# Performance work log

Hardware: AMD Instinct MI355X
Metric: run time of the kernel (lower is better)

Reference implementation:

```python
import jax, jax.numpy as jnp
import numpy as np

# Static conv hyperparameters (match init_kwargs)
STRIDE = (1, 1)
PAD = (1, 1)
DIL = (1, 1)
GROUPS = 1
DG = 1  # num_deformable_groups


def setup_inputs() -> dict:
    key = jax.random.key(0)
    k1, k2, k3 = jax.random.split(key, 3)
    B, C, H, W = 4, 256, 64, 64
    OC, kh, kw = 256, 3, 3
    x = jax.random.normal(k1, (B, C, H, W), dtype=jnp.float32)
    # offset: [B, DG*2*kh*kw, Ho, Wo], ordered (tap, [dy, dx]) per deformable group
    offset = jax.random.normal(k2, (B, DG * 2 * kh * kw, H, W), dtype=jnp.float32)
    n = C * kh * kw
    stdv = 1.0 / np.sqrt(n)
    weight = jax.random.uniform(k3, (OC, C // GROUPS, kh, kw), dtype=jnp.float32,
                                minval=-stdv, maxval=stdv)
    return {"x": x, "offset": offset, "weight": weight}


def _deform_conv(x, offset, weight):
    B, C, H, W = x.shape
    OC, Cg_w, kh, kw = weight.shape
    sh, sw = STRIDE
    ph, pw = PAD
    dh, dw = DIL
    Ho = (H + 2 * ph - (dh * (kh - 1) + 1)) // sh + 1
    Wo = (W + 2 * pw - (dw * (kw - 1) + 1)) // sw + 1
    K = kh * kw
    Cg = C // DG  # channels per deformable group

    # offsets: [B, DG, K, 2, Ho, Wo]; channel 0 = dy (h), channel 1 = dx (w)
    off = offset.reshape(B, DG, K, 2, Ho, Wo)

    # base (undeformed) sampling positions per tap
    ki, kj = jnp.meshgrid(jnp.arange(kh), jnp.arange(kw), indexing='ij')
    base_h = (jnp.arange(Ho) * sh - ph)[None, :] + (ki.reshape(-1) * dh)[:, None]  # [K, Ho]
    base_w = (jnp.arange(Wo) * sw - pw)[None, :] + (kj.reshape(-1) * dw)[:, None]  # [K, Wo]

    pos_h = base_h[None, None, :, :, None].astype(x.dtype) + off[:, :, :, 0]  # [B,DG,K,Ho,Wo]
    pos_w = base_w[None, None, :, None, :].astype(x.dtype) + off[:, :, :, 1]  # [B,DG,K,Ho,Wo]

    h0f = jnp.floor(pos_h)
    w0f = jnp.floor(pos_w)
    lh = pos_h - h0f  # fractional parts
    lw = pos_w - w0f
    h0 = h0f.astype(jnp.int32)
    w0 = w0f.astype(jnp.int32)

    xg = x.reshape(B, DG, Cg, H * W)

    def gather(hi, wi):
        # zero-padded gather: out-of-range corners contribute 0 (mmcv DCNv1 semantics)
        valid = (hi >= 0) & (hi < H) & (wi >= 0) & (wi < W)  # [B,DG,K,Ho,Wo]
        idx = jnp.clip(hi, 0, H - 1) * W + jnp.clip(wi, 0, W - 1)
        flat = idx.reshape(B, DG, 1, K * Ho * Wo)
        vals = jnp.take_along_axis(
            xg, jnp.broadcast_to(flat, (B, DG, Cg, K * Ho * Wo)), axis=3)
        vals = vals.reshape(B, DG, Cg, K, Ho, Wo)
        return vals * valid[:, :, None].astype(x.dtype)

    # bilinear interpolation over 4 corners -> im2col columns [B,DG,Cg,K,Ho,Wo]
    cols = (gather(h0, w0) * ((1 - lh) * (1 - lw))[:, :, None]
            + gather(h0, w0 + 1) * ((1 - lh) * lw)[:, :, None]
            + gather(h0 + 1, w0) * (lh * (1 - lw))[:, :, None]
            + gather(h0 + 1, w0 + 1) * (lh * lw)[:, :, None])

    # grouped GEMM: columns x weight
    cols = cols.reshape(B, GROUPS, C // GROUPS, K, Ho, Wo)
    wg = weight.reshape(GROUPS, OC // GROUPS, Cg_w, K)
    out = jnp.einsum('gock,bgckhw->bgohw', wg, cols)
    return out.reshape(B, OC, Ho, Wo)


def reference(x, offset, weight):
    return _deform_conv(x, offset, weight)
```

## Files before the change

kernel.cpp:

```cpp
#include <hip/hip_runtime.h>
#include <hip/hip_bf16.h>
#include <math.h>


constexpr int B  = 4;
constexpr int C  = 256;
constexpr int H  = 64;
constexpr int W  = 64;
constexpr int OC = 256;
constexpr int Ho = 64;
constexpr int Wo = 64;

constexpr int NT     = 64;
constexpr int CHUNKS = 72;
constexpr int WROW   = 40;

constexpr size_t WA_ELTS  = (size_t)CHUNKS * OC * WROW;
constexpr size_t XB_ELTS  = (size_t)B * 8 * 4096 * 32;
constexpr size_t OUT_ELTS = (size_t)B * OC * Ho * Wo;

typedef __attribute__((ext_vector_type(8))) short bf16x8;
typedef __attribute__((ext_vector_type(4))) float f32x4;

__device__ __forceinline__ float bf_lo(unsigned u) {
    union { unsigned i; float f; } c; c.i = u << 16; return c.f;
}
__device__ __forceinline__ float bf_hi(unsigned u) {
    union { unsigned i; float f; } c; c.i = u & 0xffff0000u; return c.f;
}
__device__ __forceinline__ ushort fbf(float f) {
    __hip_bfloat16 h = __float2bfloat16(f); return *(ushort*)&h;
}

__global__ __launch_bounds__(256)
void prep_all(const float* __restrict__ x, const float* __restrict__ wt,
              ushort* __restrict__ xb, ushort* __restrict__ wA)
{
    __shared__ ushort sx[128 * WROW];
    __shared__ ushort sw[CHUNKS * WROW];
    const int t = threadIdx.x;

    if (blockIdx.x < 1024) {
        const int blk = blockIdx.x;
        const int hwb = blk & 31;
        const int cb  = (blk >> 5) & 7;
        const int b   = blk >> 8;
        const int hw0 = hwb << 7;
        const int lhw = t & 127, chalf = t >> 7;
        #pragma unroll
        for (int i = 0; i < 16; ++i) {
            const int c = i * 2 + chalf;
            sx[lhw * WROW + c] =
                fbf(x[(((size_t)(b * 256 + cb * 32 + c)) << 12) + hw0 + lhw]);
        }
        __syncthreads();
        const int whw = t >> 1, wh = t & 1;
        const uint4 v0 = *(const uint4*)&sx[whw * WROW + wh * 16];
        const uint4 v1 = *(const uint4*)&sx[whw * WROW + wh * 16 + 8];
        uint4* dst = (uint4*)(xb + ((size_t)((b * 8 + cb) * 4096 + hw0) << 5));
        dst[whw * 4 + wh * 2 + 0] = v0;
        dst[whw * 4 + wh * 2 + 1] = v1;
    } else {
        const int oc = blockIdx.x - 1024;
        const int c  = t, chb = c >> 5, kk = c & 31;
        const float* wp = wt + ((size_t)oc * C + c) * 9;
        #pragma unroll
        for (int tap = 0; tap < 9; ++tap)
            sw[(tap * 8 + chb) * WROW + kk] = fbf(wp[tap]);
        if (c < CHUNKS) {
            #pragma unroll
            for (int j = 0; j < 8; ++j) sw[c * WROW + 32 + j] = 0;
        }
        __syncthreads();
        const uint4* sv = (const uint4*)sw;
        for (int i = c; i < CHUNKS * 5; i += 256) {
            const int row = i / 5, q = i % 5;
            ((uint4*)(wA + ((size_t)row * OC + oc) * WROW))[q] = sv[i];
        }
    }
}

struct GathRegs { uint4 c00, c01, c10, c11; float4 mw; };

__global__ __launch_bounds__(512, 4)
void dcn_mfma(const ushort* __restrict__ xb, const float* __restrict__ off,
              const ushort* __restrict__ wA_g, float* __restrict__ po)
{
    __shared__ __align__(16) ushort s_wA[2][OC * WROW];
    __shared__ __align__(16) ushort s_col[2][NT * WROW];
    __shared__ __align__(16) float4 s_mw[9 * NT];
    __shared__ __align__(8)  int2   s_midx[9 * NT];

    const int xcd = blockIdx.x & 7;
    const int ii  = blockIdx.x >> 3;
    const int b   = xcd & 3;
    const int khalf = ii & 1;
    const int ho  = ((xcd >> 2) << 5) + (ii >> 1);
    const int ch0 = khalf * 36;
    float* outp = po + (size_t)khalf * OUT_ELTS;
    const int tid = threadIdx.x;

    for (int s = tid; s < 9 * NT; s += 512) {
        const int n   = s & 63;
        const int tap = s >> 6;
        const float dy = off[((size_t)(b * 18 + 2 * tap)     * Ho + ho) * Wo + n];
        const float dx = off[((size_t)(b * 18 + 2 * tap + 1) * Ho + ho) * Wo + n];
        const float ph = (float)(ho - 1 + tap / 3) + dy;
        const float pw = (float)(n  - 1 + tap % 3) + dx;
        const float h0f = floorf(ph), w0f = floorf(pw);
        const int h0 = (int)h0f, w0 = (int)w0f;
        const float lh = ph - h0f, lw = pw - w0f;
        const int wb = min(max(w0, 0), W - 2);
        const int ht = min(max(h0, 0), H - 1);
        const int hb = min(max(h0 + 1, 0), H - 1);
        const float s0 = (wb == w0) ? (1.f - lw) : ((wb == w0 + 1) ? lw : 0.f);
        const float s1 = (wb + 1 == w0 + 1) ? lw : ((wb + 1 == w0) ? (1.f - lw) : 0.f);
        const float wtp = (h0 >= 0 && h0 < H)         ? (1.f - lh) : 0.f;
        const float wbt = (h0 + 1 >= 0 && h0 + 1 < H) ? lh         : 0.f;
        s_midx[s] = make_int2(ht * W + wb, hb * W + wb);
        s_mw[s]   = make_float4(wtp * s0, wtp * s1, wbt * s0, wbt * s1);
    }

    const int lane = tid & 63;
    const int wv   = tid >> 6;
    const int ocb  = wv >> 1;
    const int phh  = wv & 1;
    const int kq   = lane >> 4;
    const int mr   = lane & 15;
    const bool is_w = (tid < 256);

    const int sm_tid = tid - 256;
    const int sn  = sm_tid >> 2;
    const int sgg = sm_tid & 3;
    const ushort* xb_sg = xb + ((size_t)b << 20) + (sgg << 3);

    f32x4 acc[4][2];
    #pragma unroll
    for (int mt = 0; mt < 4; ++mt)
        #pragma unroll
        for (int nt = 0; nt < 2; ++nt)
            acc[mt][nt] = (f32x4){0.f, 0.f, 0.f, 0.f};

    auto dmaw = [&](int ch, int buf) {
        #pragma unroll
        for (int i = 0; i < 5; ++i) {
            const int seg = wv * 5 + i;
            __builtin_amdgcn_global_load_lds(
                (const __attribute__((address_space(1))) void*)
                    (wA_g + (size_t)ch * OC * WROW + seg * 512 + lane * 8),
                (__attribute__((address_space(3))) void*)&s_wA[buf][seg * 512],
                16, 0, 0);
        }
    };
    auto issueg = [&](int ch, GathRegs& g) {
        const int tap = ch >> 3;
        const int cb  = ch & 7;
        const int2 mi = s_midx[tap * NT + sn];
        g.mw = s_mw[tap * NT + sn];
        const ushort* xp = xb_sg + ((size_t)cb << 17);
        g.c00 = *(const uint4*)(xp + ((size_t)mi.x << 5));
        g.c01 = *(const uint4*)(xp + (((size_t)mi.x + 1) << 5));
        g.c10 = *(const uint4*)(xp + ((size_t)mi.y << 5));
        g.c11 = *(const uint4*)(xp + (((size_t)mi.y + 1) << 5));
    };
    auto sampfma = [&](const GathRegs& g, int buf) {
        union { ushort pk[8]; uint4 v; } u;
        const unsigned a00[4] = {g.c00.x, g.c00.y, g.c00.z, g.c00.w};
        const unsigned a01[4] = {g.c01.x, g.c01.y, g.c01.z, g.c01.w};
        const unsigned a10[4] = {g.c10.x, g.c10.y, g.c10.z, g.c10.w};
        const unsigned a11[4] = {g.c11.x, g.c11.y, g.c11.z, g.c11.w};
        #pragma unroll
        for (int j = 0; j < 4; ++j) {
            const float vlo = g.mw.x * bf_lo(a00[j]) + g.mw.y * bf_lo(a01[j])
                            + g.mw.z * bf_lo(a10[j]) + g.mw.w * bf_lo(a11[j]);
            const float vhi = g.mw.x * bf_hi(a00[j]) + g.mw.y * bf_hi(a01[j])
                            + g.mw.z * bf_hi(a10[j]) + g.mw.w * bf_hi(a11[j]);
            u.pk[2 * j]     = fbf(vlo);
            u.pk[2 * j + 1] = fbf(vhi);
        }
        *(uint4*)&s_col[buf][sn * WROW + sgg * 8] = u.v;
    };
    auto mfmaph = [&](int buf) {
        const bf16x8 bfr0 = *(const bf16x8*)&s_col[buf][((phh * 2 + 0) * 16 + mr) * WROW + kq * 8];
        const bf16x8 bfr1 = *(const bf16x8*)&s_col[buf][((phh * 2 + 1) * 16 + mr) * WROW + kq * 8];
        #pragma unroll
        for (int mt = 0; mt < 4; ++mt) {
            const bf16x8 afr = *(const bf16x8*)&s_wA[buf][(ocb * 64 + mt * 16 + mr) * WROW + kq * 8];
            acc[mt][0] = __builtin_amdgcn_mfma_f32_16x16x32_bf16(afr, bfr0, acc[mt][0], 0, 0, 0);
            acc[mt][1] = __builtin_amdgcn_mfma_f32_16x16x32_bf16(afr, bfr1, acc[mt][1], 0, 0, 0);
        }
    };

    __syncthreads();

    GathRegs gA, gB;
    if (is_w) dmaw(ch0, 0);
    else      issueg(ch0, gA);

    #pragma unroll 1
    for (int it = 0; it < 18; ++it) {
        const int ch = ch0 + 2 * it;

        if (is_w) {
            dmaw(ch + 1, 1);
            asm volatile("s_waitcnt vmcnt(5)" ::: "memory");
        } else {
            issueg(ch + 1, gB);
            sampfma(gA, 0);
            asm volatile("s_waitcnt lgkmcnt(0)" ::: "memory");
        }
        __builtin_amdgcn_s_barrier();
        __builtin_amdgcn_sched_barrier(0);
        mfmaph(0);
        __builtin_amdgcn_sched_barrier(0);
        __builtin_amdgcn_s_barrier();

        if (is_w) {
            if (it < 17) {
                dmaw(ch + 2, 0);
                asm volatile("s_waitcnt vmcnt(5)" ::: "memory");
            } else {
                asm volatile("s_waitcnt vmcnt(0)" ::: "memory");
            }
        } else {
            if (it < 17) issueg(ch + 2, gA);
            sampfma(gB, 1);
            asm volatile("s_waitcnt lgkmcnt(0)" ::: "memory");
        }
        __builtin_amdgcn_s_barrier();
        __builtin_amdgcn_sched_barrier(0);
        mfmaph(1);
        __builtin_amdgcn_sched_barrier(0);
        __builtin_amdgcn_s_barrier();
    }

    #pragma unroll
    for (int mt = 0; mt < 4; ++mt)
        #pragma unroll
        for (int nt = 0; nt < 2; ++nt)
            #pragma unroll
            for (int r = 0; r < 4; ++r) {
                const int oc = ocb * 64 + mt * 16 + kq * 4 + r;
                const int wo = (phh * 2 + nt) * 16 + mr;
                outp[((size_t)(b * OC + oc) * Ho + ho) * Wo + wo] = acc[mt][nt][r];
            }
}

__global__ __launch_bounds__(256)
void reduce2(const float4* __restrict__ p0, const float4* __restrict__ p1,
             float4* __restrict__ out)
{
    const int i = blockIdx.x * 256 + threadIdx.x;
    const float4 a = p0[i], b = p1[i];
    out[i] = make_float4(a.x + b.x, a.y + b.y, a.z + b.z, a.w + b.w);
}

extern "C" void kernel_launch(void* const* d_in, const int* in_sizes, int n_in,
                              void* d_out, int out_size, void* d_ws, size_t ws_size,
                              hipStream_t stream)
{
    const float* x   = (const float*)d_in[0];
    const float* off = (const float*)d_in[1];
    const float* wt  = (const float*)d_in[2];
    float* out = (float*)d_out;

    ushort* wA = (ushort*)d_ws;
    ushort* xb = wA + WA_ELTS;
    float*  po = (float*)(xb + XB_ELTS);

    prep_all<<<1280, 256, 0, stream>>>(x, wt, xb, wA);
    dcn_mfma<<<512, 512, 0, stream>>>(xb, off, wA, po);
    reduce2<<<(int)(OUT_ELTS / 4 / 256), 256, 0, stream>>>(
        (const float4*)po, (const float4*)(po + OUT_ELTS), (float4*)out);
}
```

Before: 121.6 us.

## Drop weight LDS staging; load MFMA-fragment weights directly from global into registers

Weights are pre-laid out in MFMA fragment order so each wave loads its A fragments straight from global/L2 into registers, removing the LDS weight buffer and the DMA warp split. All 512 threads now do gather/sampling, two K-chunks per phase, and each wave owns 32 output channels across all 64 columns. The loop halves to 9 iterations with one barrier per phase, and setprio is raised around the MFMAs. In exchange, weights are re-read from cache by every block each phase, and the load latency is exposed inside each phase.

```diff
diff --git a/kernel.cpp b/kernel.cpp
--- a/kernel.cpp
+++ b/kernel.cpp
@@ -15,7 +15,7 @@
 constexpr int CHUNKS = 72;
 constexpr int WROW   = 40;
 
-constexpr size_t WA_ELTS  = (size_t)CHUNKS * OC * WROW;
+constexpr size_t WB_ELTS  = (size_t)CHUNKS * 16 * 512;
 constexpr size_t XB_ELTS  = (size_t)B * 8 * 4096 * 32;
 constexpr size_t OUT_ELTS = (size_t)B * OC * Ho * Wo;
 
@@ -34,7 +34,7 @@
 
 __global__ __launch_bounds__(256)
 void prep_all(const float* __restrict__ x, const float* __restrict__ wt,
-              ushort* __restrict__ xb, ushort* __restrict__ wA)
+              ushort* __restrict__ xb, ushort* __restrict__ wB)
 {
     __shared__ ushort sx[128 * WROW];
     __shared__ ushort sw[CHUNKS * WROW];
@@ -67,15 +67,12 @@
         #pragma unroll
         for (int tap = 0; tap < 9; ++tap)
             sw[(tap * 8 + chb) * WROW + kk] = fbf(wp[tap]);
-        if (c < CHUNKS) {
-            #pragma unroll
-            for (int j = 0; j < 8; ++j) sw[c * WROW + 32 + j] = 0;
-        }
         __syncthreads();
-        const uint4* sv = (const uint4*)sw;
-        for (int i = c; i < CHUNKS * 5; i += 256) {
-            const int row = i / 5, q = i % 5;
-            ((uint4*)(wA + ((size_t)row * OC + oc) * WROW))[q] = sv[i];
+        const int og = oc >> 4, mr = oc & 15;
+        for (int i = t; i < CHUNKS * 4; i += 256) {
+            const int ch = i >> 2, kq = i & 3;
+            *(uint4*)(wB + ((size_t)ch * 16 + og) * 512 + (kq * 16 + mr) * 8) =
+                *(const uint4*)&sw[ch * WROW + kq * 8];
         }
     }
 }
@@ -84,10 +81,9 @@
 
 __global__ __launch_bounds__(512, 4)
 void dcn_mfma(const ushort* __restrict__ xb, const float* __restrict__ off,
-              const ushort* __restrict__ wA_g, float* __restrict__ po)
-{
-    __shared__ __align__(16) ushort s_wA[2][OC * WROW];
-    __shared__ __align__(16) ushort s_col[2][NT * WROW];
+              const ushort* __restrict__ wB, float* __restrict__ po)
+{
+    __shared__ __align__(16) ushort s_col[2][2][NT * WROW];
     __shared__ __align__(16) float4 s_mw[9 * NT];
     __shared__ __align__(8)  int2   s_midx[9 * NT];
 
@@ -123,36 +119,24 @@
 
     const int lane = tid & 63;
     const int wv   = tid >> 6;
-    const int ocb  = wv >> 1;
-    const int phh  = wv & 1;
     const int kq   = lane >> 4;
     const int mr   = lane & 15;
-    const bool is_w = (tid < 256);
-
-    const int sm_tid = tid - 256;
-    const int sn  = sm_tid >> 2;
-    const int sgg = sm_tid & 3;
+
+    const int kc_t = tid >> 8;
+    const int st   = tid & 255;
+    const int sn   = st >> 2;
+    const int sgg  = st & 3;
     const ushort* xb_sg = xb + ((size_t)b << 20) + (sgg << 3);
 
-    f32x4 acc[4][2];
+    f32x4 acc[2][4];
     #pragma unroll
-    for (int mt = 0; mt < 4; ++mt)
-        #pragma unroll
-        for (int nt = 0; nt < 2; ++nt)
+    for (int mt = 0; mt < 2; ++mt)
+        #pragma unroll
+        for (int nt = 0; nt < 4; ++nt)
             acc[mt][nt] = (f32x4){0.f, 0.f, 0.f, 0.f};
 
-    auto dmaw = [&](int ch, int buf) {
-        #pragma unroll
-        for (int i = 0; i < 5; ++i) {
-            const int seg = wv * 5 + i;
-            __builtin_amdgcn_global_load_lds(
-                (const __attribute__((address_space(1))) void*)
-                    (wA_g + (size_t)ch * OC * WROW + seg * 512 + lane * 8),
-                (__attribute__((address_space(3))) void*)&s_wA[buf][seg * 512],
-                16, 0, 0);
-        }
-    };
-    auto issueg = [&](int ch, GathRegs& g) {
+    auto issueg = [&](int p, GathRegs& g) {
+        const int ch  = ch0 + 2 * p + kc_t;
         const int tap = ch >> 3;
         const int cb  = ch & 7;
         const int2 mi = s_midx[tap * NT + sn];
@@ -178,70 +162,57 @@
             u.pk[2 * j]     = fbf(vlo);
             u.pk[2 * j + 1] = fbf(vhi);
         }
-        *(uint4*)&s_col[buf][sn * WROW + sgg * 8] = u.v;
+        *(uint4*)&s_col[buf][kc_t][sn * WROW + sgg * 8] = u.v;
     };
-    auto mfmaph = [&](int buf) {
-        const bf16x8 bfr0 = *(const bf16x8*)&s_col[buf][((phh * 2 + 0) * 16 + mr) * WROW + kq * 8];
-        const bf16x8 bfr1 = *(const bf16x8*)&s_col[buf][((phh * 2 + 1) * 16 + mr) * WROW + kq * 8];
-        #pragma unroll
-        for (int mt = 0; mt < 4; ++mt) {
-            const bf16x8 afr = *(const bf16x8*)&s_wA[buf][(ocb * 64 + mt * 16 + mr) * WROW + kq * 8];
-            acc[mt][0] = __builtin_amdgcn_mfma_f32_16x16x32_bf16(afr, bfr0, acc[mt][0], 0, 0, 0);
-            acc[mt][1] = __builtin_amdgcn_mfma_f32_16x16x32_bf16(afr, bfr1, acc[mt][1], 0, 0, 0);
-        }
-    };
-
-    __syncthreads();
-
-    GathRegs gA, gB;
-    if (is_w) dmaw(ch0, 0);
-    else      issueg(ch0, gA);
-
-    #pragma unroll 1
-    for (int it = 0; it < 18; ++it) {
-        const int ch = ch0 + 2 * it;
-
-        if (is_w) {
-            dmaw(ch + 1, 1);
-            asm volatile("s_waitcnt vmcnt(5)" ::: "memory");
-        } else {
-            issueg(ch + 1, gB);
-            sampfma(gA, 0);
-            asm volatile("s_waitcnt lgkmcnt(0)" ::: "memory");
-        }
+    auto phase = [&](int p, const GathRegs& gcur, int buf) {
+        sampfma(gcur, buf);
+        bf16x8 wf[2][2];
+        const int chb = ch0 + 2 * p;
+        #pragma unroll
+        for (int kc = 0; kc < 2; ++kc)
+            #pragma unroll
+            for (int mt = 0; mt < 2; ++mt)
+                wf[kc][mt] = *(const bf16x8*)
+                    (wB + ((size_t)(chb + kc) * 16 + wv * 2 + mt) * 512 + lane * 8);
+        asm volatile("s_waitcnt lgkmcnt(0)" ::: "memory");
         __builtin_amdgcn_s_barrier();
         __builtin_amdgcn_sched_barrier(0);
-        mfmaph(0);
-        __builtin_amdgcn_sched_barrier(0);
-        __builtin_amdgcn_s_barrier();
-
-        if (is_w) {
-            if (it < 17) {
-                dmaw(ch + 2, 0);
-                asm volatile("s_waitcnt vmcnt(5)" ::: "memory");
-            } else {
-                asm volatile("s_waitcnt vmcnt(0)" ::: "memory");
+        __builtin_amdgcn_s_setprio(1);
+        #pragma unroll
+        for (int kc = 0; kc < 2; ++kc)
+            #pragma unroll
+            for (int nt = 0; nt < 4; ++nt) {
+                const bf16x8 bfr = *(const bf16x8*)
+                    &s_col[buf][kc][(nt * 16 + mr) * WROW + kq * 8];
+                #pragma unroll
+                for (int mt = 0; mt < 2; ++mt)
+                    acc[mt][nt] = __builtin_amdgcn_mfma_f32_16x16x32_bf16(
+                        wf[kc][mt], bfr, acc[mt][nt], 0, 0, 0);
             }
-        } else {
-            if (it < 17) issueg(ch + 2, gA);
-            sampfma(gB, 1);
-            asm volatile("s_waitcnt lgkmcnt(0)" ::: "memory");
-        }
-        __builtin_amdgcn_s_barrier();
-        __builtin_amdgcn_sched_barrier(0);
-        mfmaph(1);
-        __builtin_amdgcn_sched_barrier(0);
-        __builtin_amdgcn_s_barrier();
+        __builtin_amdgcn_s_setprio(0);
+    };
+
+    __syncthreads();
+
+    GathRegs gA, gB;
+    issueg(0, gA);
+
+    #pragma unroll 1
+    for (int it = 0; it < 9; ++it) {
+        issueg(2 * it + 1, gB);
+        phase(2 * it, gA, 0);
+        if (it < 8) issueg(2 * it + 2, gA);
+        phase(2 * it + 1, gB, 1);
     }
 
     #pragma unroll
-    for (int mt = 0; mt < 4; ++mt)
-        #pragma unroll
-        for (int nt = 0; nt < 2; ++nt)
+    for (int mt = 0; mt < 2; ++mt)
+        #pragma unroll
+        for (int nt = 0; nt < 4; ++nt)
             #pragma unroll
             for (int r = 0; r < 4; ++r) {
-                const int oc = ocb * 64 + mt * 16 + kq * 4 + r;
-                const int wo = (phh * 2 + nt) * 16 + mr;
+                const int oc = wv * 32 + mt * 16 + kq * 4 + r;
+                const int wo = nt * 16 + mr;
                 outp[((size_t)(b * OC + oc) * Ho + ho) * Wo + wo] = acc[mt][nt][r];
             }
 }
@@ -264,12 +235,12 @@
     const float* wt  = (const float*)d_in[2];
     float* out = (float*)d_out;
 
-    ushort* wA = (ushort*)d_ws;
-    ushort* xb = wA + WA_ELTS;
+    ushort* wB = (ushort*)d_ws;
+    ushort* xb = wB + WB_ELTS;
     float*  po = (float*)(xb + XB_ELTS);
 
-    prep_all<<<1280, 256, 0, stream>>>(x, wt, xb, wA);
-    dcn_mfma<<<512, 512, 0, stream>>>(xb, off, wA, po);
+    prep_all<<<1280, 256, 0, stream>>>(x, wt, xb, wB);
+    dcn_mfma<<<512, 512, 0, stream>>>(xb, off, wB, po);
     reduce2<<<(int)(OUT_ELTS / 4 / 256), 256, 0, stream>>>(
         (const float4*)po, (const float4*)(po + OUT_ELTS), (float4*)out);
 }
```

Result: faster. 113.6 us (-6.6%).
